# Kernel optimization log

Hardware: AMD Instinct MI355X
Metric: run time of the kernel (lower is better)

## Reference

```python
import jax, jax.numpy as jnp
import numpy as np

N = 100000   # nodes
E = 640000   # edges
D = 128      # feature dim
G = 512      # graphs in the batch


def setup_inputs() -> dict:
    key = jax.random.key(0)
    ks = jax.random.split(key, 6)
    x = jax.random.normal(ks[0], (N, D), dtype=jnp.float32)
    edge_index = jax.random.randint(ks[1], (2, E), 0, N, dtype=jnp.int32)
    batch = jnp.sort(jax.random.randint(ks[2], (N,), 0, G, dtype=jnp.int32))
    scale = 1.0 / np.sqrt(D)
    W0 = jax.random.normal(ks[3], (D, D), dtype=jnp.float32) * scale
    W1 = jax.random.normal(ks[4], (D, D), dtype=jnp.float32) * scale
    W2 = jax.random.normal(ks[5], (D, D), dtype=jnp.float32) * scale
    return {"x": x, "edge_index": edge_index, "batch": batch,
            "W0": W0, "W1": W1, "W2": W2}


def gcn_conv(x, W, row, col, n):
    """GCNConv (bias=False): x' = D^-1/2 (A + I) D^-1/2 (x @ W).
    row/col already include self-loops."""
    xw = x @ W                                              # [N, D]
    deg = jax.ops.segment_sum(jnp.ones_like(col, dtype=x.dtype), col,
                              num_segments=n)               # [N]
    dinv = jnp.where(deg > 0, jax.lax.rsqrt(deg), 0.0)
    norm = dinv[row] * dinv[col]                            # [E+N]
    msgs = norm[:, None] * xw[row]                          # gather + scale
    return jax.ops.segment_sum(msgs, col, num_segments=n)   # scatter-add


def reference(x, edge_index, batch, W0, W1, W2):
    n = x.shape[0]
    loops = jnp.arange(n, dtype=edge_index.dtype)
    row = jnp.concatenate([edge_index[0], loops])
    col = jnp.concatenate([edge_index[1], loops])
    # conv_layers[:-1] (no activation between them in forward)
    x = gcn_conv(x, W0, row, col, n)
    x = gcn_conv(x, W1, row, col, n)
    x = jax.nn.leaky_relu(x, negative_slope=0.01)
    x = gcn_conv(x, W2, row, col, n)
    # global_add_pool over graph ids
    return jax.ops.segment_sum(x, batch, num_segments=G)    # [G, D]
```

## Files before the change

kernel.cpp:

```cpp
#include <hip/hip_runtime.h>
#include <hip/hip_bf16.h>
#include <type_traits>

#define FEAT 128

typedef unsigned int uint32;
typedef unsigned short ushort16;
typedef __attribute__((ext_vector_type(8))) short short8;
typedef __attribute__((ext_vector_type(4))) float v4f;

__device__ __forceinline__ ushort16 f2bf(float f) {
    uint32 u = __float_as_uint(f);
    u += 0x7fffu + ((u >> 16) & 1u);
    return (ushort16)(u >> 16);
}
__device__ __forceinline__ float bflo(uint32 u) { return __uint_as_float(u << 16); }
__device__ __forceinline__ float bfhi(uint32 u) { return __uint_as_float(u & 0xffff0000u); }

__global__ void hist_kernel(const int* __restrict__ col, int* __restrict__ counts, int E) {
    int e = blockIdx.x * 256 + threadIdx.x;
    if (e < E) atomicAdd(&counts[col[e]], 1);
}

__global__ __launch_bounds__(256) void scan_part(const int* __restrict__ counts,
                                                 int* __restrict__ bsum, int n) {
    __shared__ int s[256];
    int base = blockIdx.x * 1024;
    int t = threadIdx.x;
    int v = 0;
#pragma unroll
    for (int i = 0; i < 4; i++) {
        int idx = base + t * 4 + i;
        if (idx < n) v += counts[idx];
    }
    s[t] = v;
    __syncthreads();
    for (int o = 128; o > 0; o >>= 1) {
        if (t < o) s[t] += s[t + o];
        __syncthreads();
    }
    if (t == 0) bsum[blockIdx.x] = s[0];
}

__global__ void scan_bsum(int* __restrict__ bsum, int nb) {
    __shared__ int s[128];
    int t = threadIdx.x;
    int v0 = (t < nb) ? bsum[t] : 0;
    s[t] = v0;
    __syncthreads();
    for (int o = 1; o < 128; o <<= 1) {
        int v = (t >= o) ? s[t - o] : 0;
        __syncthreads();
        s[t] += v;
        __syncthreads();
    }
    if (t < nb) bsum[t] = s[t] - v0;
}

__global__ __launch_bounds__(256) void scan_final(const int* __restrict__ counts,
                                                  const int* __restrict__ bsum,
                                                  int* __restrict__ off, int* __restrict__ nxt,
                                                  float* __restrict__ dinv, int n) {
    __shared__ int s[256];
    int base = blockIdx.x * 1024;
    int t = threadIdx.x;
    int c[4];
    int sum = 0;
#pragma unroll
    for (int i = 0; i < 4; i++) {
        int idx = base + t * 4 + i;
        c[i] = (idx < n) ? counts[idx] : 0;
        sum += c[i];
    }
    int v0 = sum;
    s[t] = sum;
    __syncthreads();
    for (int o = 1; o < 256; o <<= 1) {
        int v = (t >= o) ? s[t - o] : 0;
        __syncthreads();
        s[t] += v;
        __syncthreads();
    }
    int excl = s[t] - v0 + bsum[blockIdx.x];
#pragma unroll
    for (int i = 0; i < 4; i++) {
        int idx = base + t * 4 + i;
        if (idx < n) {
            off[idx] = excl;
            nxt[idx] = excl;
            dinv[idx] = rsqrtf((float)(c[i] + 1));
        }
        excl += c[i];
    }
    if (blockIdx.x == gridDim.x - 1 && t == 255) off[n] = excl;
}

__global__ void fill_kernel(const int* __restrict__ row, const int* __restrict__ col,
                            const float* __restrict__ dinv, int* __restrict__ nxt,
                            int* __restrict__ src, float* __restrict__ snrm, int E) {
    int e = blockIdx.x * 256 + threadIdx.x;
    if (e < E) {
        int c = col[e], r = row[e];
        int p = atomicAdd(&nxt[c], 1);
        src[p] = r;
        snrm[p] = dinv[r];
    }
}

__global__ __launch_bounds__(256) void cvt_w_kernel(const float* __restrict__ W0,
                                                    const float* __restrict__ W1,
                                                    const float* __restrict__ W2,
                                                    ushort16* __restrict__ Wt) {
    int id = blockIdx.x * 256 + threadIdx.x;
    if (id >= 3 * 16384) return;
    int m = id >> 14;
    int o = id & 16383;
    int ncol = o >> 7;
    int k = o & 127;
    const float* W = (m == 0) ? W0 : (m == 1) ? W1 : W2;
    Wt[id] = f2bf(W[(size_t)k * FEAT + ncol]);
}

template <typename T>
__global__ __launch_bounds__(256) void gemm_mfma(const T* __restrict__ A,
                                                 const ushort16* __restrict__ Wt,
                                                 ushort16* __restrict__ Ch, int n) {
    __shared__ ushort16 sW[128 * 136];
    __shared__ ushort16 sOut[4 * 2048];

    const int t = threadIdx.x;
    {
        int r = t >> 1, half = t & 1;
        const ushort16* s = Wt + (size_t)r * 128 + half * 64;
        ushort16* d = sW + r * 136 + half * 64;
#pragma unroll
        for (int i = 0; i < 8; i++)
            *(uint4*)(d + i * 8) = *(const uint4*)(s + i * 8);
    }
    __syncthreads();

    const int w = t >> 6;
    const int lane = t & 63;
    const int quad = lane >> 4;
    const int l16 = lane & 15;
    const int rowBase = blockIdx.x * 64 + w * 16;

    short8 a[4];
    const int arow = rowBase + l16;
    if (arow < n) {
        if constexpr (std::is_same<T, float>::value) {
#pragma unroll
            for (int ks = 0; ks < 4; ks++) {
                const float* ap = A + (size_t)arow * FEAT + quad * 8 + ks * 32;
                float4 f0 = *(const float4*)ap;
                float4 f1 = *(const float4*)(ap + 4);
                short8 v;
                v[0] = f2bf(f0.x); v[1] = f2bf(f0.y); v[2] = f2bf(f0.z); v[3] = f2bf(f0.w);
                v[4] = f2bf(f1.x); v[5] = f2bf(f1.y); v[6] = f2bf(f1.z); v[7] = f2bf(f1.w);
                a[ks] = v;
            }
        } else {
            const ushort16* ap = A + (size_t)arow * FEAT + quad * 8;
#pragma unroll
            for (int ks = 0; ks < 4; ks++) a[ks] = *(const short8*)(ap + ks * 32);
        }
    } else {
#pragma unroll
        for (int ks = 0; ks < 4; ks++) a[ks] = (short8)0;
    }

    v4f acc[8];
#pragma unroll
    for (int ct = 0; ct < 8; ct++) acc[ct] = (v4f)0.f;

#pragma unroll
    for (int ct = 0; ct < 8; ct++) {
        const ushort16* bp = sW + (ct * 16 + l16) * 136 + quad * 8;
#pragma unroll
        for (int ks = 0; ks < 4; ks++) {
            short8 b = *(const short8*)(bp + ks * 32);
            acc[ct] = __builtin_amdgcn_mfma_f32_16x16x32_bf16(a[ks], b, acc[ct], 0, 0, 0);
        }
    }

    ushort16* so = sOut + w * 2048;
#pragma unroll
    for (int ct = 0; ct < 8; ct++) {
#pragma unroll
        for (int r = 0; r < 4; r++) {
            int rloc = quad * 4 + r;
            int chSt = ((ct * 2) + (l16 >> 3)) ^ rloc;
            so[rloc * 128 + chSt * 8 + (l16 & 7)] = f2bf(acc[ct][r]);
        }
    }
#pragma unroll
    for (int p = 0; p < 4; p++) {
        int idx = p * 64 + lane;
        int lr = idx >> 4;
        int m = idx & 15;
        int row = rowBase + lr;
        if (row < n)
            *(uint4*)(Ch + (size_t)row * FEAT + m * 8) =
                *(const uint4*)(so + lr * 128 + ((m ^ lr) * 8));
    }
}

__global__ __launch_bounds__(256) void gather_kernel(const int* __restrict__ off,
                                                     const int* __restrict__ src,
                                                     const float* __restrict__ snrm,
                                                     const float* __restrict__ dinv,
                                                     const ushort16* __restrict__ XWh,
                                                     ushort16* __restrict__ Hh,
                                                     float* __restrict__ Hf,
                                                     int n, int mode) {
    int node = blockIdx.x * 4 + (threadIdx.x >> 6);
    if (node >= n) return;
    int lane = threadIdx.x & 63;
    int grp = lane >> 4;
    int l16 = lane & 15;
    float dc = dinv[node];
    const uint4* table = (const uint4*)XWh;

    float acc[8];
    if (grp == 0) {
        uint4 v = table[(size_t)node * 16 + l16];
        float w0 = dc * dc;
        acc[0] = w0 * bflo(v.x); acc[1] = w0 * bfhi(v.x);
        acc[2] = w0 * bflo(v.y); acc[3] = w0 * bfhi(v.y);
        acc[4] = w0 * bflo(v.z); acc[5] = w0 * bfhi(v.z);
        acc[6] = w0 * bflo(v.w); acc[7] = w0 * bfhi(v.w);
    } else {
#pragma unroll
        for (int j = 0; j < 8; j++) acc[j] = 0.f;
    }

    int s = off[node], e = off[node + 1];
    for (int i = s + grp; i < e; i += 4) {
        int r = src[i];
        float nrm = dc * snrm[i];
        uint4 u = table[(size_t)r * 16 + l16];
        acc[0] += nrm * bflo(u.x); acc[1] += nrm * bfhi(u.x);
        acc[2] += nrm * bflo(u.y); acc[3] += nrm * bfhi(u.y);
        acc[4] += nrm * bflo(u.z); acc[5] += nrm * bfhi(u.z);
        acc[6] += nrm * bflo(u.w); acc[7] += nrm * bfhi(u.w);
    }

#pragma unroll
    for (int j = 0; j < 8; j++) {
        acc[j] += __shfl_xor(acc[j], 16);
        acc[j] += __shfl_xor(acc[j], 32);
    }

    if (mode == 2) {
        if (grp < 2) {
            float4 o = (grp == 0) ? make_float4(acc[0], acc[1], acc[2], acc[3])
                                  : make_float4(acc[4], acc[5], acc[6], acc[7]);
            *(float4*)(Hf + (size_t)node * FEAT + l16 * 8 + grp * 4) = o;
        }
    } else {
        if (mode == 1) {
#pragma unroll
            for (int j = 0; j < 8; j++) acc[j] = (acc[j] >= 0.f) ? acc[j] : 0.01f * acc[j];
        }
        if (grp == 0) {
            uint4 o;
            o.x = (uint32)f2bf(acc[0]) | ((uint32)f2bf(acc[1]) << 16);
            o.y = (uint32)f2bf(acc[2]) | ((uint32)f2bf(acc[3]) << 16);
            o.z = (uint32)f2bf(acc[4]) | ((uint32)f2bf(acc[5]) << 16);
            o.w = (uint32)f2bf(acc[6]) | ((uint32)f2bf(acc[7]) << 16);
            *(uint4*)(Hh + (size_t)node * FEAT + l16 * 8) = o;
        }
    }
}

__global__ __launch_bounds__(128) void pool_kernel(const float* __restrict__ H,
                                                   const int* __restrict__ batch,
                                                   float* __restrict__ out, int n) {
    int t = threadIdx.x;
    int i0 = blockIdx.x * 64;
    if (i0 >= n) return;
    int i1 = min(i0 + 64, n);
    float acc = 0.f;
    int g = batch[i0];
    for (int i = i0; i < i1; i++) {
        int b = batch[i];
        if (b != g) {
            atomicAdd(&out[(size_t)g * FEAT + t], acc);
            acc = 0.f;
            g = b;
        }
        acc += H[(size_t)i * FEAT + t];
    }
    atomicAdd(&out[(size_t)g * FEAT + t], acc);
}

extern "C" void kernel_launch(void* const* d_in, const int* in_sizes, int n_in,
                              void* d_out, int out_size, void* d_ws, size_t ws_size,
                              hipStream_t stream) {
    const float* x = (const float*)d_in[0];
    const int* ei = (const int*)d_in[1];
    const int* batch = (const int*)d_in[2];
    const float* W0 = (const float*)d_in[3];
    const float* W1 = (const float*)d_in[4];
    const float* W2 = (const float*)d_in[5];
    float* out = (float*)d_out;

    const int N = in_sizes[0] / FEAT;
    const int E = in_sizes[1] / 2;

    const int* rowI = ei;
    const int* colI = ei + E;

    char* ws = (char*)d_ws;
    auto take = [&](size_t bytes) {
        char* p = ws;
        ws += (bytes + 15) & ~(size_t)15;
        return p;
    };
    int* counts   = (int*)take((size_t)N * 4);
    int* off      = (int*)take((size_t)(N + 1) * 4);
    int* nxt      = (int*)take((size_t)N * 4);
    float* dinv   = (float*)take((size_t)N * 4);
    int* bsum     = (int*)take(128 * 4);
    int* src      = (int*)take((size_t)E * 4);
    float* snrm   = (float*)take((size_t)E * 4);
    ushort16* Wt  = (ushort16*)take((size_t)3 * 16384 * 2);
    ushort16* Hh  = (ushort16*)take((size_t)N * FEAT * 2);
    ushort16* XWh = (ushort16*)take((size_t)N * FEAT * 2);
    float* Hf = (float*)Hh;

    const int nb = (N + 1023) / 1024;
    const int eb = (E + 255) / 256;

    cvt_w_kernel<<<(3 * 16384 + 255) / 256, 256, 0, stream>>>(W0, W1, W2, Wt);

    hipMemsetAsync(counts, 0, (size_t)N * 4, stream);
    hist_kernel<<<eb, 256, 0, stream>>>(colI, counts, E);
    scan_part<<<nb, 256, 0, stream>>>(counts, bsum, N);
    scan_bsum<<<1, 128, 0, stream>>>(bsum, nb);
    scan_final<<<nb, 256, 0, stream>>>(counts, bsum, off, nxt, dinv, N);
    fill_kernel<<<eb, 256, 0, stream>>>(rowI, colI, dinv, nxt, src, snrm, E);

    const int gemmBlocks = (N + 63) / 64;
    const int gatBlocks = (N + 3) / 4;

    gemm_mfma<float><<<gemmBlocks, 256, 0, stream>>>(x, Wt, XWh, N);
    gather_kernel<<<gatBlocks, 256, 0, stream>>>(off, src, snrm, dinv, XWh, Hh, nullptr, N, 0);
    gemm_mfma<ushort16><<<gemmBlocks, 256, 0, stream>>>(Hh, Wt + 16384, XWh, N);
    gather_kernel<<<gatBlocks, 256, 0, stream>>>(off, src, snrm, dinv, XWh, Hh, nullptr, N, 1);
    gemm_mfma<ushort16><<<gemmBlocks, 256, 0, stream>>>(Hh, Wt + 2 * 16384, XWh, N);
    {
        float* HfSep = (float*)take((size_t)N * FEAT * 4);
        gather_kernel<<<gatBlocks, 256, 0, stream>>>(off, src, snrm, dinv, XWh, nullptr, HfSep, N, 2);
        hipMemsetAsync(out, 0, (size_t)out_size * 4, stream);
        pool_kernel<<<(N + 63) / 64, 128, 0, stream>>>(HfSep, batch, out, N);
    }
}
```

Baseline: 374.1 us.

## Persistent GEMM with register-resident weights, packed edge records, wider gather lanes

The GEMM becomes persistent: 512 blocks each load all bf16 weight fragments into registers once and loop over 16-row tiles. It swaps the MFMA operand order so results are written straight to global memory, dropping the shared-memory output staging. Edge source index and normalisation are packed into one uint2 record, so each edge needs one load instead of two. The gather now uses 8 edge groups of 8 lanes, each lane loading 32 bytes per row, which adds a shuffle stage and raises register pressure.

New measurement: 389.2 us. +4.0%, slower.

```diff
diff --git a/kernel.cpp b/kernel.cpp
--- a/kernel.cpp
+++ b/kernel.cpp
@@ -97,13 +97,12 @@
 
 __global__ void fill_kernel(const int* __restrict__ row, const int* __restrict__ col,
                             const float* __restrict__ dinv, int* __restrict__ nxt,
-                            int* __restrict__ src, float* __restrict__ snrm, int E) {
+                            uint2* __restrict__ erec, int E) {
     int e = blockIdx.x * 256 + threadIdx.x;
     if (e < E) {
         int c = col[e], r = row[e];
         int p = atomicAdd(&nxt[c], 1);
-        src[p] = r;
-        snrm[p] = dinv[r];
+        erec[p] = make_uint2((uint32)r, __float_as_uint(dinv[r]));
     }
 }
 
@@ -122,11 +121,10 @@
 }
 
 template <typename T>
-__global__ __launch_bounds__(256) void gemm_mfma(const T* __restrict__ A,
-                                                 const ushort16* __restrict__ Wt,
-                                                 ushort16* __restrict__ Ch, int n) {
+__global__ __launch_bounds__(256, 2) void gemm_mfma(const T* __restrict__ A,
+                                                    const ushort16* __restrict__ Wt,
+                                                    ushort16* __restrict__ Ch, int n) {
     __shared__ ushort16 sW[128 * 136];
-    __shared__ ushort16 sOut[4 * 2048];
 
     const int t = threadIdx.x;
     {
@@ -143,71 +141,64 @@
     const int lane = t & 63;
     const int quad = lane >> 4;
     const int l16 = lane & 15;
-    const int rowBase = blockIdx.x * 64 + w * 16;
-
-    short8 a[4];
-    const int arow = rowBase + l16;
-    if (arow < n) {
-        if constexpr (std::is_same<T, float>::value) {
-#pragma unroll
-            for (int ks = 0; ks < 4; ks++) {
-                const float* ap = A + (size_t)arow * FEAT + quad * 8 + ks * 32;
-                float4 f0 = *(const float4*)ap;
-                float4 f1 = *(const float4*)(ap + 4);
-                short8 v;
-                v[0] = f2bf(f0.x); v[1] = f2bf(f0.y); v[2] = f2bf(f0.z); v[3] = f2bf(f0.w);
-                v[4] = f2bf(f1.x); v[5] = f2bf(f1.y); v[6] = f2bf(f1.z); v[7] = f2bf(f1.w);
-                a[ks] = v;
+
+    short8 bw[8][4];
+#pragma unroll
+    for (int ct = 0; ct < 8; ct++) {
+        const ushort16* bp = sW + (ct * 16 + l16) * 136 + quad * 8;
+#pragma unroll
+        for (int ks = 0; ks < 4; ks++) bw[ct][ks] = *(const short8*)(bp + ks * 32);
+    }
+
+    const int nTiles = (n + 15) >> 4;
+    for (int tile = blockIdx.x * 4 + w; tile < nTiles; tile += gridDim.x * 4) {
+        const int row = tile * 16 + l16;
+        short8 a[4];
+        if (row < n) {
+            if constexpr (std::is_same<T, float>::value) {
+#pragma unroll
+                for (int ks = 0; ks < 4; ks++) {
+                    const float* ap = A + (size_t)row * FEAT + quad * 8 + ks * 32;
+                    float4 f0 = *(const float4*)ap;
+                    float4 f1 = *(const float4*)(ap + 4);
+                    short8 v;
+                    v[0] = f2bf(f0.x); v[1] = f2bf(f0.y); v[2] = f2bf(f0.z); v[3] = f2bf(f0.w);
+                    v[4] = f2bf(f1.x); v[5] = f2bf(f1.y); v[6] = f2bf(f1.z); v[7] = f2bf(f1.w);
+                    a[ks] = v;
+                }
+            } else {
+                const ushort16* ap = A + (size_t)row * FEAT + quad * 8;
+#pragma unroll
+                for (int ks = 0; ks < 4; ks++) a[ks] = *(const short8*)(ap + ks * 32);
             }
         } else {
-            const ushort16* ap = A + (size_t)arow * FEAT + quad * 8;
-#pragma unroll
-            for (int ks = 0; ks < 4; ks++) a[ks] = *(const short8*)(ap + ks * 32);
-        }
-    } else {
-#pragma unroll
-        for (int ks = 0; ks < 4; ks++) a[ks] = (short8)0;
-    }
-
-    v4f acc[8];
-#pragma unroll
-    for (int ct = 0; ct < 8; ct++) acc[ct] = (v4f)0.f;
-
-#pragma unroll
-    for (int ct = 0; ct < 8; ct++) {
-        const ushort16* bp = sW + (ct * 16 + l16) * 136 + quad * 8;
-#pragma unroll
-        for (int ks = 0; ks < 4; ks++) {
-            short8 b = *(const short8*)(bp + ks * 32);
-            acc[ct] = __builtin_amdgcn_mfma_f32_16x16x32_bf16(a[ks], b, acc[ct], 0, 0, 0);
-        }
-    }
-
-    ushort16* so = sOut + w * 2048;
-#pragma unroll
-    for (int ct = 0; ct < 8; ct++) {
-#pragma unroll
-        for (int r = 0; r < 4; r++) {
-            int rloc = quad * 4 + r;
-            int chSt = ((ct * 2) + (l16 >> 3)) ^ rloc;
-            so[rloc * 128 + chSt * 8 + (l16 & 7)] = f2bf(acc[ct][r]);
-        }
-    }
-#pragma unroll
-    for (int p = 0; p < 4; p++) {
-        int idx = p * 64 + lane;
-        int lr = idx >> 4;
-        int m = idx & 15;
-        int row = rowBase + lr;
-        if (row < n)
-            *(uint4*)(Ch + (size_t)row * FEAT + m * 8) =
-                *(const uint4*)(so + lr * 128 + ((m ^ lr) * 8));
+#pragma unroll
+            for (int ks = 0; ks < 4; ks++) a[ks] = (short8)0;
+        }
+
+        v4f acc[8];
+#pragma unroll
+        for (int ct = 0; ct < 8; ct++) acc[ct] = (v4f)0.f;
+#pragma unroll
+        for (int ct = 0; ct < 8; ct++)
+#pragma unroll
+            for (int ks = 0; ks < 4; ks++)
+                acc[ct] = __builtin_amdgcn_mfma_f32_16x16x32_bf16(bw[ct][ks], a[ks], acc[ct], 0, 0, 0);
+
+        if (row < n) {
+#pragma unroll
+            for (int ct = 0; ct < 8; ct++) {
+                uint2 o;
+                o.x = (uint32)f2bf(acc[ct][0]) | ((uint32)f2bf(acc[ct][1]) << 16);
+                o.y = (uint32)f2bf(acc[ct][2]) | ((uint32)f2bf(acc[ct][3]) << 16);
+                *(uint2*)(Ch + (size_t)row * FEAT + ct * 16 + quad * 4) = o;
+            }
+        }
     }
 }
 
 __global__ __launch_bounds__(256) void gather_kernel(const int* __restrict__ off,
-                                                     const int* __restrict__ src,
-                                                     const float* __restrict__ snrm,
+                                                     const uint2* __restrict__ erec,
                                                      const float* __restrict__ dinv,
                                                      const ushort16* __restrict__ XWh,
                                                      ushort16* __restrict__ Hh,
@@ -216,59 +207,79 @@
     int node = blockIdx.x * 4 + (threadIdx.x >> 6);
     if (node >= n) return;
     int lane = threadIdx.x & 63;
-    int grp = lane >> 4;
-    int l16 = lane & 15;
+    int grp = lane >> 3;
+    int l8 = lane & 7;
     float dc = dinv[node];
     const uint4* table = (const uint4*)XWh;
 
-    float acc[8];
+    float acc[16];
     if (grp == 0) {
-        uint4 v = table[(size_t)node * 16 + l16];
+        size_t b = (size_t)node * 16 + l8 * 2;
+        uint4 v0 = table[b], v1 = table[b + 1];
         float w0 = dc * dc;
-        acc[0] = w0 * bflo(v.x); acc[1] = w0 * bfhi(v.x);
-        acc[2] = w0 * bflo(v.y); acc[3] = w0 * bfhi(v.y);
-        acc[4] = w0 * bflo(v.z); acc[5] = w0 * bfhi(v.z);
-        acc[6] = w0 * bflo(v.w); acc[7] = w0 * bfhi(v.w);
+        acc[0] = w0 * bflo(v0.x); acc[1] = w0 * bfhi(v0.x);
+        acc[2] = w0 * bflo(v0.y); acc[3] = w0 * bfhi(v0.y);
+        acc[4] = w0 * bflo(v0.z); acc[5] = w0 * bfhi(v0.z);
+        acc[6] = w0 * bflo(v0.w); acc[7] = w0 * bfhi(v0.w);
+        acc[8] = w0 * bflo(v1.x); acc[9] = w0 * bfhi(v1.x);
+        acc[10] = w0 * bflo(v1.y); acc[11] = w0 * bfhi(v1.y);
+        acc[12] = w0 * bflo(v1.z); acc[13] = w0 * bfhi(v1.z);
+        acc[14] = w0 * bflo(v1.w); acc[15] = w0 * bfhi(v1.w);
     } else {
 #pragma unroll
-        for (int j = 0; j < 8; j++) acc[j] = 0.f;
+        for (int j = 0; j < 16; j++) acc[j] = 0.f;
     }
 
     int s = off[node], e = off[node + 1];
-    for (int i = s + grp; i < e; i += 4) {
-        int r = src[i];
-        float nrm = dc * snrm[i];
-        uint4 u = table[(size_t)r * 16 + l16];
-        acc[0] += nrm * bflo(u.x); acc[1] += nrm * bfhi(u.x);
-        acc[2] += nrm * bflo(u.y); acc[3] += nrm * bfhi(u.y);
-        acc[4] += nrm * bflo(u.z); acc[5] += nrm * bfhi(u.z);
-        acc[6] += nrm * bflo(u.w); acc[7] += nrm * bfhi(u.w);
-    }
-
-#pragma unroll
-    for (int j = 0; j < 8; j++) {
+    for (int i = s + grp; i < e; i += 8) {
+        uint2 er = erec[i];
+        float nrm = dc * __uint_as_float(er.y);
+        size_t rb = (size_t)er.x * 16 + l8 * 2;
+        uint4 u0 = table[rb], u1 = table[rb + 1];
+        acc[0] += nrm * bflo(u0.x); acc[1] += nrm * bfhi(u0.x);
+        acc[2] += nrm * bflo(u0.y); acc[3] += nrm * bfhi(u0.y);
+        acc[4] += nrm * bflo(u0.z); acc[5] += nrm * bfhi(u0.z);
+        acc[6] += nrm * bflo(u0.w); acc[7] += nrm * bfhi(u0.w);
+        acc[8] += nrm * bflo(u1.x); acc[9] += nrm * bfhi(u1.x);
+        acc[10] += nrm * bflo(u1.y); acc[11] += nrm * bfhi(u1.y);
+        acc[12] += nrm * bflo(u1.z); acc[13] += nrm * bfhi(u1.z);
+        acc[14] += nrm * bflo(u1.w); acc[15] += nrm * bfhi(u1.w);
+    }
+
+#pragma unroll
+    for (int j = 0; j < 16; j++) {
+        acc[j] += __shfl_xor(acc[j], 8);
         acc[j] += __shfl_xor(acc[j], 16);
         acc[j] += __shfl_xor(acc[j], 32);
     }
 
     if (mode == 2) {
-        if (grp < 2) {
-            float4 o = (grp == 0) ? make_float4(acc[0], acc[1], acc[2], acc[3])
-                                  : make_float4(acc[4], acc[5], acc[6], acc[7]);
-            *(float4*)(Hf + (size_t)node * FEAT + l16 * 8 + grp * 4) = o;
+        float* hp = Hf + (size_t)node * FEAT + l8 * 16;
+        if (grp == 0) {
+            *(float4*)(hp + 0) = make_float4(acc[0], acc[1], acc[2], acc[3]);
+            *(float4*)(hp + 4) = make_float4(acc[4], acc[5], acc[6], acc[7]);
+        } else if (grp == 1) {
+            *(float4*)(hp + 8) = make_float4(acc[8], acc[9], acc[10], acc[11]);
+            *(float4*)(hp + 12) = make_float4(acc[12], acc[13], acc[14], acc[15]);
         }
     } else {
         if (mode == 1) {
 #pragma unroll
-            for (int j = 0; j < 8; j++) acc[j] = (acc[j] >= 0.f) ? acc[j] : 0.01f * acc[j];
+            for (int j = 0; j < 16; j++) acc[j] = (acc[j] >= 0.f) ? acc[j] : 0.01f * acc[j];
         }
         if (grp == 0) {
-            uint4 o;
-            o.x = (uint32)f2bf(acc[0]) | ((uint32)f2bf(acc[1]) << 16);
-            o.y = (uint32)f2bf(acc[2]) | ((uint32)f2bf(acc[3]) << 16);
-            o.z = (uint32)f2bf(acc[4]) | ((uint32)f2bf(acc[5]) << 16);
-            o.w = (uint32)f2bf(acc[6]) | ((uint32)f2bf(acc[7]) << 16);
-            *(uint4*)(Hh + (size_t)node * FEAT + l16 * 8) = o;
+            uint4 o0, o1;
+            o0.x = (uint32)f2bf(acc[0]) | ((uint32)f2bf(acc[1]) << 16);
+            o0.y = (uint32)f2bf(acc[2]) | ((uint32)f2bf(acc[3]) << 16);
+            o0.z = (uint32)f2bf(acc[4]) | ((uint32)f2bf(acc[5]) << 16);
+            o0.w = (uint32)f2bf(acc[6]) | ((uint32)f2bf(acc[7]) << 16);
+            o1.x = (uint32)f2bf(acc[8]) | ((uint32)f2bf(acc[9]) << 16);
+            o1.y = (uint32)f2bf(acc[10]) | ((uint32)f2bf(acc[11]) << 16);
+            o1.z = (uint32)f2bf(acc[12]) | ((uint32)f2bf(acc[13]) << 16);
+            o1.w = (uint32)f2bf(acc[14]) | ((uint32)f2bf(acc[15]) << 16);
+            ushort16* hp = Hh + (size_t)node * FEAT + l8 * 16;
+            *(uint4*)(hp + 0) = o0;
+            *(uint4*)(hp + 8) = o1;
         }
     }
 }
@@ -322,12 +333,11 @@
     int* nxt      = (int*)take((size_t)N * 4);
     float* dinv   = (float*)take((size_t)N * 4);
     int* bsum     = (int*)take(128 * 4);
-    int* src      = (int*)take((size_t)E * 4);
-    float* snrm   = (float*)take((size_t)E * 4);
+    uint2* erec   = (uint2*)take((size_t)E * 8);
     ushort16* Wt  = (ushort16*)take((size_t)3 * 16384 * 2);
     ushort16* Hh  = (ushort16*)take((size_t)N * FEAT * 2);
     ushort16* XWh = (ushort16*)take((size_t)N * FEAT * 2);
-    float* Hf = (float*)Hh;
+    float* Hf     = (float*)take((size_t)N * FEAT * 4);
 
     const int nb = (N + 1023) / 1024;
     const int eb = (E + 255) / 256;
@@ -339,20 +349,18 @@
     scan_part<<<nb, 256, 0, stream>>>(counts, bsum, N);
     scan_bsum<<<1, 128, 0, stream>>>(bsum, nb);
     scan_final<<<nb, 256, 0, stream>>>(counts, bsum, off, nxt, dinv, N);
-    fill_kernel<<<eb, 256, 0, stream>>>(rowI, colI, dinv, nxt, src, snrm, E);
-
-    const int gemmBlocks = (N + 63) / 64;
+    fill_kernel<<<eb, 256, 0, stream>>>(rowI, colI, dinv, nxt, erec, E);
+
+    const int gemmBlocks = 512;
     const int gatBlocks = (N + 3) / 4;
 
     gemm_mfma<float><<<gemmBlocks, 256, 0, stream>>>(x, Wt, XWh, N);
-    gather_kernel<<<gatBlocks, 256, 0, stream>>>(off, src, snrm, dinv, XWh, Hh, nullptr, N, 0);
+    gather_kernel<<<gatBlocks, 256, 0, stream>>>(off, erec, dinv, XWh, Hh, nullptr, N, 0);
     gemm_mfma<ushort16><<<gemmBlocks, 256, 0, stream>>>(Hh, Wt + 16384, XWh, N);
-    gather_kernel<<<gatBlocks, 256, 0, stream>>>(off, src, snrm, dinv, XWh, Hh, nullptr, N, 1);
+    gather_kernel<<<gatBlocks, 256, 0, stream>>>(off, erec, dinv, XWh, Hh, nullptr, N, 1);
     gemm_mfma<ushort16><<<gemmBlocks, 256, 0, stream>>>(Hh, Wt + 2 * 16384, XWh, N);
-    {
-        float* HfSep = (float*)take((size_t)N * FEAT * 4);
-        gather_kernel<<<gatBlocks, 256, 0, stream>>>(off, src, snrm, dinv, XWh, nullptr, HfSep, N, 2);
-        hipMemsetAsync(out, 0, (size_t)out_size * 4, stream);
-        pool_kernel<<<(N + 63) / 64, 128, 0, stream>>>(HfSep, batch, out, N);
-    }
-}
+    gather_kernel<<<gatBlocks, 256, 0, stream>>>(off, erec, dinv, XWh, nullptr, Hf, N, 2);
+
+    hipMemsetAsync(out, 0, (size_t)out_size * 4, stream);
+    pool_kernel<<<(N + 63) / 64, 128, 0, stream>>>(Hf, batch, out, N);
+}
```
